# Kernel tuning notes

Hardware: AMD Instinct MI355X
Metric: run time of the kernel (lower is better)

The kernel has to match this reference:

```python
import jax, jax.numpy as jnp
import numpy as np

N_GRAPHS = 64
ATOMS = 32
N = N_GRAPHS * ATOMS          # 2048 total nodes
HID = 128                     # num_hidden_feature
FEAT = 64                     # num_ligand_atom_feature
D1_MIN, D1_MAX, D1_BINS = 0.0, 10.0, 32   # dist_one_hot_param1
D2_BINS = 64                  # dist_one_hot_param2[-1]
N_DENSE = 3
GAMMA = 10.0                  # SoftOneHot gaussian width
NEG = -9e15


def _linear_init(key, n_out, n_in):
    kw, kb = jax.random.split(key)
    bound = 1.0 / np.sqrt(n_in)
    W = jax.random.uniform(kw, (n_out, n_in), jnp.float32, -bound, bound)
    b = jax.random.uniform(kb, (n_out,), jnp.float32, -bound, bound)
    return W, b


def setup_inputs() -> dict:
    key = jax.random.key(0)
    ks = jax.random.split(key, 12)
    h = jax.random.normal(ks[0], (N, HID), jnp.float32)
    pos = jax.random.normal(ks[1], (N, 3), jnp.float32) * 3.0
    next_type = jax.random.normal(ks[2], (N_GRAPHS, FEAT), jnp.float32)
    batch = (jnp.arange(N, dtype=jnp.int32) // ATOMS)  # sorted segment ids

    W_emb = _linear_init(ks[3], HID, FEAT)[0]          # embedding has no bias
    W_qkv, b_qkv = _linear_init(ks[4], 3 * HID, HID)
    W_b, b_b = _linear_init(ks[5], 1, HID)
    W_g, b_g = _linear_init(ks[6], 1, HID)
    W_t, b_t = _linear_init(ks[7], 1, D1_BINS)
    dims = list(np.linspace(HID, D2_BINS, N_DENSE + 1).astype(int))  # [128,106,85,64]
    W_d0, b_d0 = _linear_init(ks[8], dims[1], dims[0])
    W_d1, b_d1 = _linear_init(ks[9], dims[2], dims[1])
    W_d2, b_d2 = _linear_init(ks[10], dims[3], dims[2])
    return {"h": h, "pos": pos, "next_type": next_type, "batch": batch,
            "W_emb": W_emb, "W_qkv": W_qkv, "b_qkv": b_qkv,
            "W_b": W_b, "b_b": b_b, "W_g": W_g, "b_g": b_g,
            "W_t": W_t, "b_t": b_t,
            "W_d0": W_d0, "b_d0": b_d0, "W_d1": W_d1, "b_d1": b_d1,
            "W_d2": W_d2, "b_d2": b_d2}


def reference(h, pos, next_type, batch, W_emb, W_qkv, b_qkv, W_b, b_b,
              W_g, b_g, W_t, b_t, W_d0, b_d0, W_d1, b_d1, W_d2, b_d2):
    # length per graph (scatter_add of ones)
    length = jax.ops.segment_sum(jnp.ones((N,), jnp.float32), batch,
                                 num_segments=N_GRAPHS)
    # dist_embed = h * embedding(next_type)[batch]
    x = h * (next_type @ W_emb.T)[batch]

    sqrt_len = (length ** -0.5)[batch]                 # [N]
    # block-diagonal mask (batch is sorted, so equality == block diag)
    mask = batch[:, None] == batch[None, :]            # [N,N] bool

    # cdist + SoftOneHot (gaussian soft one-hot over linspace centers)
    sq = jnp.sum((pos[:, None, :] - pos[None, :, :]) ** 2, -1)
    d = jnp.sqrt(jnp.maximum(sq, 1e-12))               # [N,N]
    centers = jnp.linspace(D1_MIN, D1_MAX, D1_BINS)
    intra = jnp.exp(-GAMMA * (d[..., None] - centers) ** 2)  # [N,N,BINS]
    t = jnp.einsum('ijk,k->ij', intra, W_t[0]) + b_t[0]      # t_proj.squeeze(-1)

    qkv = x @ W_qkv.T + b_qkv
    q, k, v = jnp.split(qkv, 3, axis=-1)
    b_bias = x @ W_b.T + b_b                           # [N,1], per-row bias
    g = jax.nn.sigmoid(x @ W_g.T + b_g)                # [N,1] gate

    logits = (q @ k.T) * sqrt_len[:, None] + b_bias + t
    logits = jnp.where(mask, logits, NEG)
    attn = jax.nn.softmax(logits, axis=-1)
    vals = (attn @ v) * g + x                          # gated residual

    # dense head: SiLU between layers, none after last
    y = jax.nn.silu(vals @ W_d0.T + b_d0)
    y = jax.nn.silu(y @ W_d1.T + b_d1)
    y = y @ W_d2.T + b_d2
    return jax.nn.log_softmax(y, axis=-1)
```

## Files before the change

### kernel.cpp

```cpp
#include <hip/hip_runtime.h>

typedef __bf16 bf16_t;
typedef __bf16 bf16x8 __attribute__((ext_vector_type(8)));
typedef float  f32x4  __attribute__((ext_vector_type(4)));

#define HPAD   132
#define LDSPAD 136
#define VPAD   40

#define WQ_OFF   0
#define WD0_OFF  49152
#define WD1_OFF  63488
#define WD2_OFF  75776
#define WS_ELEMS 81920

__global__ __launch_bounds__(256)
void preconvert(const float* __restrict__ Wqkv, const float* __restrict__ Wd0,
                const float* __restrict__ Wd1, const float* __restrict__ Wd2,
                bf16_t* __restrict__ ws) {
    int i = blockIdx.x * 256 + threadIdx.x;
    if (i >= WS_ELEMS) return;
    if (i < WD0_OFF) {
        ws[i] = (bf16_t)Wqkv[i];
    } else if (i < WD1_OFF) {
        int j = i - WD0_OFF, r = j >> 7, c = j & 127;
        ws[i] = (r < 106) ? (bf16_t)Wd0[r * 128 + c] : (bf16_t)0.0f;
    } else if (i < WD2_OFF) {
        int j = i - WD1_OFF, r = j >> 7, c = j & 127;
        ws[i] = (r < 85 && c < 106) ? (bf16_t)Wd1[r * 106 + c] : (bf16_t)0.0f;
    } else {
        int j = i - WD2_OFF, r = j / 96, c = j - r * 96;
        ws[i] = (c < 85) ? (bf16_t)Wd2[r * 85 + c] : (bf16_t)0.0f;
    }
}

__global__ __launch_bounds__(1024)
void nextdist_fused(const float* __restrict__ h,
                    const float* __restrict__ pos,
                    const float* __restrict__ ntype,
                    const float* __restrict__ Wemb,
                    const float* __restrict__ bqkv,
                    const float* __restrict__ Wg,
                    const float* __restrict__ bg,
                    const float* __restrict__ Wt,
                    const float* __restrict__ bt,
                    const float* __restrict__ bd0,
                    const float* __restrict__ bd1,
                    const float* __restrict__ bd2,
                    const bf16_t* __restrict__ ws,
                    float* __restrict__ out)
{
    __shared__ __align__(16) float  s_hf[32 * HPAD];
    __shared__ __align__(16) bf16_t s_x [32 * LDSPAD];
    __shared__ __align__(16) bf16_t s_q [32 * LDSPAD];
    __shared__ __align__(16) bf16_t s_k [32 * LDSPAD];
    __shared__ __align__(16) bf16_t s_vT[128 * VPAD];
    __shared__ __align__(16) bf16_t s_p [32 * VPAD];
    __shared__ __align__(16) float  s_t [32 * 33];
    __shared__ __align__(16) float  s_y2[32 * 66];
    __shared__ float s_emb[128];
    __shared__ float s_nt[64];
    __shared__ float s_pos[96];
    __shared__ float s_wt[32];
    __shared__ float s_wg[128];
    __shared__ float s_gate[32];

    const bf16_t* __restrict__ Wqkvb = ws + WQ_OFF;
    const bf16_t* __restrict__ Wd0b  = ws + WD0_OFF;
    const bf16_t* __restrict__ Wd1b  = ws + WD1_OFF;
    const bf16_t* __restrict__ Wd2b  = ws + WD2_OFF;

    const int tid  = threadIdx.x;
    const int wave = tid >> 6;
    const int lane = tid & 63;
    const int quad = lane >> 4;
    const int l16  = lane & 15;
    const int g    = blockIdx.x;
    const int base = g * 32;

    {
        int a = tid >> 5, ch = tid & 31;
        *(float4*)&s_hf[a * HPAD + ch * 4] = *(const float4*)&h[(base + a) * 128 + ch * 4];
    }
    if (tid < 96)  s_pos[tid] = pos[base * 3 + tid];
    if (tid < 64)  s_nt[tid]  = ntype[g * 64 + tid];
    if (tid < 32)  s_wt[tid]  = Wt[tid];
    if (tid < 128) s_wg[tid]  = Wg[tid];
    __syncthreads();

    {
        int o = tid >> 3, p = tid & 7;
        float acc = 0.0f;
#pragma unroll
        for (int f = p * 8; f < p * 8 + 8; ++f) acc += Wemb[o * 64 + f] * s_nt[f];
#pragma unroll
        for (int s = 1; s < 8; s <<= 1) acc += __shfl_xor(acc, s, 64);
        if (p == 0) s_emb[o] = acc;
    }
    __syncthreads();

    for (int c = tid; c < 4096; c += 1024) {
        int a = c >> 7, f = c & 127;
        s_x[a * LDSPAD + f] = (bf16_t)(s_hf[a * HPAD + f] * s_emb[f]);
    }
    if (tid < 256) {
        int r = tid >> 3, p = tid & 7;
        float acc = 0.0f;
#pragma unroll
        for (int f = p * 16; f < p * 16 + 16; ++f) acc += s_hf[r * HPAD + f] * s_emb[f] * s_wg[f];
#pragma unroll
        for (int s = 1; s < 8; s <<= 1) acc += __shfl_xor(acc, s, 64);
        if (p == 0) s_gate[r] = 1.0f / (1.0f + __expf(-(acc + bg[0])));
    }
    __syncthreads();

    for (int t = wave; t < 48; t += 16) {
        int nt = t >> 1, mt = t & 1;
        int o  = nt * 16 + l16;
        const bf16_t* wrow = &Wqkvb[o * 128];
        f32x4 acc = {0.f, 0.f, 0.f, 0.f};
#pragma unroll
        for (int ks = 0; ks < 4; ++ks) {
            bf16x8 av = *(const bf16x8*)&s_x[(mt * 16 + l16) * LDSPAD + ks * 32 + quad * 8];
            bf16x8 bv = *(const bf16x8*)&wrow[ks * 32 + quad * 8];
            acc = __builtin_amdgcn_mfma_f32_16x16x32_bf16(av, bv, acc, 0, 0, 0);
        }
        float bias = bqkv[o];
#pragma unroll
        for (int r = 0; r < 4; ++r) {
            int a = mt * 16 + quad * 4 + r;
            float val = acc[r] + bias;
            if (o < 128)      s_q[a * LDSPAD + o]         = (bf16_t)val;
            else if (o < 256) s_k[a * LDSPAD + (o - 128)] = (bf16_t)val;
            else              s_vT[(o - 256) * VPAD + a]  = (bf16_t)val;
        }
    }

    {
        const float bt0 = bt[0];
        int i = tid >> 5, j = tid & 31;
        float dx = s_pos[i * 3 + 0] - s_pos[j * 3 + 0];
        float dy = s_pos[i * 3 + 1] - s_pos[j * 3 + 1];
        float dz = s_pos[i * 3 + 2] - s_pos[j * 3 + 2];
        float d  = sqrtf(fmaxf(dx * dx + dy * dy + dz * dz, 1e-12f));
        float acc = bt0;
#pragma unroll
        for (int kk = 0; kk < 32; ++kk) {
            float u = d - (float)kk * (10.0f / 31.0f);
            acc += s_wt[kk] * __expf(-10.0f * u * u);
        }
        s_t[i * 33 + j] = acc;
    }
    __syncthreads();

    if (wave < 4) {
        int mt = wave >> 1, nt = wave & 1;
        f32x4 acc = {0.f, 0.f, 0.f, 0.f};
#pragma unroll
        for (int ks = 0; ks < 4; ++ks) {
            bf16x8 av = *(const bf16x8*)&s_q[(mt * 16 + l16) * LDSPAD + ks * 32 + quad * 8];
            bf16x8 bv = *(const bf16x8*)&s_k[(nt * 16 + l16) * LDSPAD + ks * 32 + quad * 8];
            acc = __builtin_amdgcn_mfma_f32_16x16x32_bf16(av, bv, acc, 0, 0, 0);
        }
#pragma unroll
        for (int r = 0; r < 4; ++r) {
            int i = mt * 16 + quad * 4 + r, j = nt * 16 + l16;
            s_t[i * 33 + j] = acc[r] * 0.17677669529663687f + s_t[i * 33 + j];
        }
    }
    __syncthreads();

    if (tid < 256) {
        int r = tid >> 3, sub = tid & 7;
        float v[4]; float mx = -1e30f;
#pragma unroll
        for (int c = 0; c < 4; ++c) { v[c] = s_t[r * 33 + sub * 4 + c]; mx = fmaxf(mx, v[c]); }
#pragma unroll
        for (int s = 1; s < 8; s <<= 1) mx = fmaxf(mx, __shfl_xor(mx, s, 64));
        float sum = 0.0f;
#pragma unroll
        for (int c = 0; c < 4; ++c) { v[c] = __expf(v[c] - mx); sum += v[c]; }
#pragma unroll
        for (int s = 1; s < 8; s <<= 1) sum += __shfl_xor(sum, s, 64);
        float inv = 1.0f / sum;
#pragma unroll
        for (int c = 0; c < 4; ++c) s_p[r * VPAD + sub * 4 + c] = (bf16_t)(v[c] * inv);
    }
    __syncthreads();

    {
        int nt = wave >> 1, mt = wave & 1;
        bf16x8 av = *(const bf16x8*)&s_p[(mt * 16 + l16) * VPAD + quad * 8];
        bf16x8 bv = *(const bf16x8*)&s_vT[(nt * 16 + l16) * VPAD + quad * 8];
        f32x4 acc = {0.f, 0.f, 0.f, 0.f};
        acc = __builtin_amdgcn_mfma_f32_16x16x32_bf16(av, bv, acc, 0, 0, 0);
#pragma unroll
        for (int r = 0; r < 4; ++r) {
            int a = mt * 16 + quad * 4 + r, f = nt * 16 + l16;
            float val = acc[r] * s_gate[a] + s_hf[a * HPAD + f] * s_emb[f];
            s_x[a * LDSPAD + f] = (bf16_t)val;
        }
    }
    if (tid < 512) {
        int a = tid >> 4, c = 112 + (tid & 15);
        s_q[a * LDSPAD + c] = (bf16_t)0.0f;
    }
    __syncthreads();

    if (wave < 14) {
        int nt = wave >> 1, mt = wave & 1;
        int o = nt * 16 + l16;
        const bf16_t* wrow = &Wd0b[o * 128];
        f32x4 acc = {0.f, 0.f, 0.f, 0.f};
#pragma unroll
        for (int ks = 0; ks < 4; ++ks) {
            bf16x8 av = *(const bf16x8*)&s_x[(mt * 16 + l16) * LDSPAD + ks * 32 + quad * 8];
            bf16x8 bv = *(const bf16x8*)&wrow[ks * 32 + quad * 8];
            acc = __builtin_amdgcn_mfma_f32_16x16x32_bf16(av, bv, acc, 0, 0, 0);
        }
        float bias = (o < 106) ? bd0[o] : 0.0f;
#pragma unroll
        for (int r = 0; r < 4; ++r) {
            int a = mt * 16 + quad * 4 + r;
            float val = acc[r] + bias;
            s_q[a * LDSPAD + o] = (bf16_t)(val / (1.0f + __expf(-val)));
        }
    }
    __syncthreads();

    if (wave < 12) {
        int nt = wave >> 1, mt = wave & 1;
        int o = nt * 16 + l16;
        const bf16_t* wrow = &Wd1b[o * 128];
        f32x4 acc = {0.f, 0.f, 0.f, 0.f};
#pragma unroll
        for (int ks = 0; ks < 4; ++ks) {
            bf16x8 av = *(const bf16x8*)&s_q[(mt * 16 + l16) * LDSPAD + ks * 32 + quad * 8];
            bf16x8 bv = *(const bf16x8*)&wrow[ks * 32 + quad * 8];
            acc = __builtin_amdgcn_mfma_f32_16x16x32_bf16(av, bv, acc, 0, 0, 0);
        }
        float bias = (o < 85) ? bd1[o] : 0.0f;
#pragma unroll
        for (int r = 0; r < 4; ++r) {
            int a = mt * 16 + quad * 4 + r;
            float val = acc[r] + bias;
            s_k[a * LDSPAD + o] = (bf16_t)(val / (1.0f + __expf(-val)));
        }
    }
    __syncthreads();

    if (wave < 8) {
        int nt = wave >> 1, mt = wave & 1;
        int o = nt * 16 + l16;
        const bf16_t* wrow = &Wd2b[o * 96];
        f32x4 acc = {0.f, 0.f, 0.f, 0.f};
#pragma unroll
        for (int ks = 0; ks < 3; ++ks) {
            bf16x8 av = *(const bf16x8*)&s_k[(mt * 16 + l16) * LDSPAD + ks * 32 + quad * 8];
            bf16x8 bv = *(const bf16x8*)&wrow[ks * 32 + quad * 8];
            acc = __builtin_amdgcn_mfma_f32_16x16x32_bf16(av, bv, acc, 0, 0, 0);
        }
        float bias = bd2[o];
#pragma unroll
        for (int r = 0; r < 4; ++r) {
            int a = mt * 16 + quad * 4 + r;
            s_y2[a * 66 + o] = acc[r] + bias;
        }
    }
    __syncthreads();

    if (tid < 256) {
        int r = tid >> 3, sub = tid & 7;
        float v[8]; float mx = -1e30f;
#pragma unroll
        for (int c = 0; c < 8; ++c) { v[c] = s_y2[r * 66 + sub * 8 + c]; mx = fmaxf(mx, v[c]); }
#pragma unroll
        for (int s = 1; s < 8; s <<= 1) mx = fmaxf(mx, __shfl_xor(mx, s, 64));
        float sum = 0.0f;
#pragma unroll
        for (int c = 0; c < 8; ++c) sum += __expf(v[c] - mx);
#pragma unroll
        for (int s = 1; s < 8; s <<= 1) sum += __shfl_xor(sum, s, 64);
        float lse = mx + __logf(sum);
#pragma unroll
        for (int c = 0; c < 8; ++c)
            out[(base + r) * 64 + sub * 8 + c] = v[c] - lse;
    }
}

extern "C" void kernel_launch(void* const* d_in, const int* in_sizes, int n_in,
                              void* d_out, int out_size, void* d_ws, size_t ws_size,
                              hipStream_t stream) {
    const float* h     = (const float*)d_in[0];
    const float* pos   = (const float*)d_in[1];
    const float* ntype = (const float*)d_in[2];
    const float* Wemb  = (const float*)d_in[4];
    const float* Wqkv  = (const float*)d_in[5];
    const float* bqkv  = (const float*)d_in[6];
    const float* Wg    = (const float*)d_in[9];
    const float* bg    = (const float*)d_in[10];
    const float* Wt    = (const float*)d_in[11];
    const float* bt    = (const float*)d_in[12];
    const float* Wd0   = (const float*)d_in[13];
    const float* bd0   = (const float*)d_in[14];
    const float* Wd1   = (const float*)d_in[15];
    const float* bd1   = (const float*)d_in[16];
    const float* Wd2   = (const float*)d_in[17];
    const float* bd2   = (const float*)d_in[18];
    float* out = (float*)d_out;
    bf16_t* ws = (bf16_t*)d_ws;

    preconvert<<<dim3((WS_ELEMS + 255) / 256), dim3(256), 0, stream>>>(Wqkv, Wd0, Wd1, Wd2, ws);
    nextdist_fused<<<dim3(64), dim3(1024), 0, stream>>>(
        h, pos, ntype, Wemb, bqkv, Wg, bg, Wt, bt,
        bd0, bd1, bd2, ws, out);
}
```

Measured before the change: 109.4 us.

## Prefetch weight fragments into registers ahead of barriers to hide global latency

```diff
diff --git a/kernel.cpp b/kernel.cpp
--- a/kernel.cpp
+++ b/kernel.cpp
@@ -86,13 +86,31 @@
     if (tid < 64)  s_nt[tid]  = ntype[g * 64 + tid];
     if (tid < 32)  s_wt[tid]  = Wt[tid];
     if (tid < 128) s_wg[tid]  = Wg[tid];
-    __syncthreads();
-
+
+    float4 we0, we1;
     {
         int o = tid >> 3, p = tid & 7;
-        float acc = 0.0f;
-#pragma unroll
-        for (int f = p * 8; f < p * 8 + 8; ++f) acc += Wemb[o * 64 + f] * s_nt[f];
+        we0 = *(const float4*)&Wemb[o * 64 + p * 8];
+        we1 = *(const float4*)&Wemb[o * 64 + p * 8 + 4];
+    }
+    bf16x8 wq[3][4]; float bq3[3];
+#pragma unroll
+    for (int t3 = 0; t3 < 3; ++t3) {
+        int t = wave + t3 * 16;
+        int o = (t >> 1) * 16 + l16;
+        const bf16_t* wrow = &Wqkvb[o * 128];
+#pragma unroll
+        for (int ks = 0; ks < 4; ++ks)
+            wq[t3][ks] = *(const bf16x8*)&wrow[ks * 32 + quad * 8];
+        bq3[t3] = bqkv[o];
+    }
+    __syncthreads();
+
+    {
+        int o = tid >> 3, p = tid & 7;
+        const float* nt8 = &s_nt[p * 8];
+        float acc = we0.x * nt8[0] + we0.y * nt8[1] + we0.z * nt8[2] + we0.w * nt8[3]
+                  + we1.x * nt8[4] + we1.y * nt8[5] + we1.z * nt8[6] + we1.w * nt8[7];
 #pragma unroll
         for (int s = 1; s < 8; s <<= 1) acc += __shfl_xor(acc, s, 64);
         if (p == 0) s_emb[o] = acc;
@@ -114,26 +132,40 @@
     }
     __syncthreads();
 
-    for (int t = wave; t < 48; t += 16) {
-        int nt = t >> 1, mt = t & 1;
-        int o  = nt * 16 + l16;
-        const bf16_t* wrow = &Wqkvb[o * 128];
-        f32x4 acc = {0.f, 0.f, 0.f, 0.f};
-#pragma unroll
-        for (int ks = 0; ks < 4; ++ks) {
-            bf16x8 av = *(const bf16x8*)&s_x[(mt * 16 + l16) * LDSPAD + ks * 32 + quad * 8];
-            bf16x8 bv = *(const bf16x8*)&wrow[ks * 32 + quad * 8];
-            acc = __builtin_amdgcn_mfma_f32_16x16x32_bf16(av, bv, acc, 0, 0, 0);
-        }
-        float bias = bqkv[o];
-#pragma unroll
-        for (int r = 0; r < 4; ++r) {
-            int a = mt * 16 + quad * 4 + r;
-            float val = acc[r] + bias;
-            if (o < 128)      s_q[a * LDSPAD + o]         = (bf16_t)val;
-            else if (o < 256) s_k[a * LDSPAD + (o - 128)] = (bf16_t)val;
-            else              s_vT[(o - 256) * VPAD + a]  = (bf16_t)val;
-        }
+    {
+        int mt = wave & 1;
+        bf16x8 av[4];
+#pragma unroll
+        for (int ks = 0; ks < 4; ++ks)
+            av[ks] = *(const bf16x8*)&s_x[(mt * 16 + l16) * LDSPAD + ks * 32 + quad * 8];
+#pragma unroll
+        for (int t3 = 0; t3 < 3; ++t3) {
+            int t = wave + t3 * 16;
+            int o = (t >> 1) * 16 + l16;
+            f32x4 acc = {0.f, 0.f, 0.f, 0.f};
+#pragma unroll
+            for (int ks = 0; ks < 4; ++ks)
+                acc = __builtin_amdgcn_mfma_f32_16x16x32_bf16(av[ks], wq[t3][ks], acc, 0, 0, 0);
+            float bias = bq3[t3];
+#pragma unroll
+            for (int r = 0; r < 4; ++r) {
+                int a = mt * 16 + quad * 4 + r;
+                float val = acc[r] + bias;
+                if (o < 128)      s_q[a * LDSPAD + o]         = (bf16_t)val;
+                else if (o < 256) s_k[a * LDSPAD + (o - 128)] = (bf16_t)val;
+                else              s_vT[(o - 256) * VPAD + a]  = (bf16_t)val;
+            }
+        }
+    }
+
+    bf16x8 w8[4]; float b8v = 0.0f;
+    const int oD = (wave >> 1) * 16 + l16;
+    if (wave < 14) {
+        const bf16_t* wrow = &Wd0b[oD * 128];
+#pragma unroll
+        for (int ks = 0; ks < 4; ++ks)
+            w8[ks] = *(const bf16x8*)&wrow[ks * 32 + quad * 8];
+        b8v = (oD < 106) ? bd0[oD] : 0.0f;
     }
 
     {
@@ -205,66 +237,71 @@
         int a = tid >> 4, c = 112 + (tid & 15);
         s_q[a * LDSPAD + c] = (bf16_t)0.0f;
     }
-    __syncthreads();
-
+
+    bf16x8 w9[4]; float b9v = 0.0f;
+    if (wave < 12) {
+        const bf16_t* wrow = &Wd1b[oD * 128];
+#pragma unroll
+        for (int ks = 0; ks < 4; ++ks)
+            w9[ks] = *(const bf16x8*)&wrow[ks * 32 + quad * 8];
+        b9v = (oD < 85) ? bd1[oD] : 0.0f;
+    }
+    __syncthreads();
+
+    bf16x8 w10[3]; float b10v = 0.0f;
+    if (wave < 8) {
+        const bf16_t* wrow = &Wd2b[oD * 96];
+#pragma unroll
+        for (int ks = 0; ks < 3; ++ks)
+            w10[ks] = *(const bf16x8*)&wrow[ks * 32 + quad * 8];
+        b10v = bd2[oD];
+    }
     if (wave < 14) {
-        int nt = wave >> 1, mt = wave & 1;
-        int o = nt * 16 + l16;
-        const bf16_t* wrow = &Wd0b[o * 128];
+        int mt = wave & 1;
         f32x4 acc = {0.f, 0.f, 0.f, 0.f};
 #pragma unroll
         for (int ks = 0; ks < 4; ++ks) {
             bf16x8 av = *(const bf16x8*)&s_x[(mt * 16 + l16) * LDSPAD + ks * 32 + quad * 8];
-            bf16x8 bv = *(const bf16x8*)&wrow[ks * 32 + quad * 8];
-            acc = __builtin_amdgcn_mfma_f32_16x16x32_bf16(av, bv, acc, 0, 0, 0);
-        }
-        float bias = (o < 106) ? bd0[o] : 0.0f;
+            acc = __builtin_amdgcn_mfma_f32_16x16x32_bf16(av, w8[ks], acc, 0, 0, 0);
+        }
 #pragma unroll
         for (int r = 0; r < 4; ++r) {
             int a = mt * 16 + quad * 4 + r;
-            float val = acc[r] + bias;
-            s_q[a * LDSPAD + o] = (bf16_t)(val / (1.0f + __expf(-val)));
+            float val = acc[r] + b8v;
+            s_q[a * LDSPAD + oD] = (bf16_t)(val / (1.0f + __expf(-val)));
         }
     }
     __syncthreads();
 
     if (wave < 12) {
-        int nt = wave >> 1, mt = wave & 1;
-        int o = nt * 16 + l16;
-        const bf16_t* wrow = &Wd1b[o * 128];
+        int mt = wave & 1;
         f32x4 acc = {0.f, 0.f, 0.f, 0.f};
 #pragma unroll
         for (int ks = 0; ks < 4; ++ks) {
             bf16x8 av = *(const bf16x8*)&s_q[(mt * 16 + l16) * LDSPAD + ks * 32 + quad * 8];
-            bf16x8 bv = *(const bf16x8*)&wrow[ks * 32 + quad * 8];
-            acc = __builtin_amdgcn_mfma_f32_16x16x32_bf16(av, bv, acc, 0, 0, 0);
-        }
-        float bias = (o < 85) ? bd1[o] : 0.0f;
+            acc = __builtin_amdgcn_mfma_f32_16x16x32_bf16(av, w9[ks], acc, 0, 0, 0);
+        }
 #pragma unroll
         for (int r = 0; r < 4; ++r) {
             int a = mt * 16 + quad * 4 + r;
-            float val = acc[r] + bias;
-            s_k[a * LDSPAD + o] = (bf16_t)(val / (1.0f + __expf(-val)));
+            float val = acc[r] + b9v;
+            s_k[a * LDSPAD + oD] = (bf16_t)(val / (1.0f + __expf(-val)));
         }
     }
     __syncthreads();
 
     if (wave < 8) {
-        int nt = wave >> 1, mt = wave & 1;
-        int o = nt * 16 + l16;
-        const bf16_t* wrow = &Wd2b[o * 96];
+        int mt = wave & 1;
         f32x4 acc = {0.f, 0.f, 0.f, 0.f};
 #pragma unroll
         for (int ks = 0; ks < 3; ++ks) {
             bf16x8 av = *(const bf16x8*)&s_k[(mt * 16 + l16) * LDSPAD + ks * 32 + quad * 8];
-            bf16x8 bv = *(const bf16x8*)&wrow[ks * 32 + quad * 8];
-            acc = __builtin_amdgcn_mfma_f32_16x16x32_bf16(av, bv, acc, 0, 0, 0);
-        }
-        float bias = bd2[o];
+            acc = __builtin_amdgcn_mfma_f32_16x16x32_bf16(av, w10[ks], acc, 0, 0, 0);
+        }
 #pragma unroll
         for (int r = 0; r < 4; ++r) {
             int a = mt * 16 + quad * 4 + r;
-            s_y2[a * 66 + o] = acc[r] + bias;
+            s_y2[a * 66 + oD] = acc[r] + b10v;
         }
     }
     __syncthreads();
@@ -282,9 +319,11 @@
 #pragma unroll
         for (int s = 1; s < 8; s <<= 1) sum += __shfl_xor(sum, s, 64);
         float lse = mx + __logf(sum);
-#pragma unroll
-        for (int c = 0; c < 8; ++c)
-            out[(base + r) * 64 + sub * 8 + c] = v[c] - lse;
+        float4 o0 = make_float4(v[0] - lse, v[1] - lse, v[2] - lse, v[3] - lse);
+        float4 o1 = make_float4(v[4] - lse, v[5] - lse, v[6] - lse, v[7] - lse);
+        float* op = &out[(base + r) * 64 + sub * 8];
+        *(float4*)op = o0;
+        *(float4*)(op + 4) = o1;
     }
 }
 
```

Result: faster. 105.2 us (-3.8%).
